# Optimization experiments

Hardware: AMD Instinct MI355X
Metric: run time of the kernel (lower is better)

Reference implementation:

```python
import jax, jax.numpy as jnp
import numpy as np

N_NODES = 100000
N_EDGES = 3200000
HID = 16
MP_ROUNDS = 3


def _mlp(w1, b1, w2, b2, x):
    # channels-first MLP applied per edge/node: x is [C_in, E]
    h = jax.nn.relu(w1 @ x + b1[:, None])
    return w2 @ h + b2[:, None]


def setup_inputs() -> dict:
    key = jax.random.key(0)
    ks = jax.random.split(key, 20)
    s = lambda k, shp: jax.random.normal(k, shp, dtype=jnp.float32) * 0.1
    inp = {
        "nodes": jax.random.normal(ks[0], (N_NODES,), dtype=jnp.float32),
        "edges_init": jax.random.normal(ks[1], (N_EDGES,), dtype=jnp.float32),
        "senders": jax.random.randint(ks[2], (N_EDGES,), 0, N_NODES, dtype=jnp.int32),
        "receivers": jax.random.randint(ks[3], (N_EDGES,), 0, N_NODES, dtype=jnp.int32),
        # EdgeEncoder: 1 -> HID -> HID
        "enc_w1": s(ks[4], (HID, 1)), "enc_b1": jnp.zeros((HID,), jnp.float32),
        "enc_w2": s(ks[5], (HID, HID)), "enc_b2": jnp.zeros((HID,), jnp.float32),
        # Node update MLP: (1 + 2*HID) -> HID -> 1  (shared across rounds)
        "node_w1": s(ks[6], (HID, 1 + 2 * HID)), "node_b1": jnp.zeros((HID,), jnp.float32),
        "node_w2": s(ks[7], (1, HID)), "node_b2": jnp.zeros((1,), jnp.float32),
        # Edge update MLP: (HID + 2) -> HID -> HID  (shared across rounds)
        "edge_w1": s(ks[8], (HID, HID + 2)), "edge_b1": jnp.zeros((HID,), jnp.float32),
        "edge_w2": s(ks[9], (HID, HID)), "edge_b2": jnp.zeros((HID,), jnp.float32),
        # EdgeDecoder: HID -> HID -> 1
        "dec_w1": s(ks[10], (HID, HID)), "dec_b1": jnp.zeros((HID,), jnp.float32),
        "dec_w2": s(ks[11], (1, HID)), "dec_b2": jnp.zeros((1,), jnp.float32),
        "alpha": jnp.float32(0.1),
    }
    return inp


def reference(nodes, edges_init, senders, receivers,
              enc_w1, enc_b1, enc_w2, enc_b2,
              node_w1, node_b1, node_w2, node_b2,
              edge_w1, edge_b1, edge_w2, edge_b2,
              dec_w1, dec_b1, dec_w2, dec_b2, alpha):
    n_nodes = nodes.shape[0]
    norm = jnp.abs(edges_init).max()
    e = edges_init / norm                      # [E]
    e = _mlp(enc_w1, enc_b1, enc_w2, enc_b2, e[None, :])   # [HID, E]
    for _ in range(MP_ROUNDS):                 # shared-weight MP blocks
        # gather/scatter: aggregate edge features to nodes
        agg_s = jax.ops.segment_sum(e.T, senders, num_segments=n_nodes).T     # [HID, N]
        agg_r = jax.ops.segment_sum(e.T, receivers, num_segments=n_nodes).T   # [HID, N]
        node_in = jnp.concatenate([nodes[None, :], agg_s, agg_r], axis=0)     # [1+2H, N]
        nodes = _mlp(node_w1, node_b1, node_w2, node_b2, node_in)[0]          # [N]
        edge_in = jnp.concatenate([e, nodes[senders][None, :], nodes[receivers][None, :]], axis=0)  # [H+2, E]
        e = _mlp(edge_w1, edge_b1, edge_w2, edge_b2, edge_in)                 # [HID, E]
    e = _mlp(dec_w1, dec_b1, dec_w2, dec_b2, e)[0]          # [E]
    low_tri_data = edges_init + alpha * (e * norm)          # L = L + alpha*GNN(L)
    return low_tri_data
```

## Files before the change

kernel.cpp:

```cpp
#include <hip/hip_runtime.h>
#include <hip/hip_bf16.h>

#define N_NODES 100000
#define N_EDGES 3200000
#define HID 16
#define NB 256
#define NPB 391
#define SCAP 15360
#define RCAP 15360
#define FDEPTH 32
#define LCAP1 8704
#define LCAP2 26624

static constexpr int BLK = 256;

__device__ __forceinline__ float frelu(float x) { return fmaxf(x, 0.f); }
__device__ __forceinline__ float bflo(unsigned int u) {
  return __uint_as_float(u << 16);
}
__device__ __forceinline__ float bfhi(unsigned int u) {
  return __uint_as_float(u & 0xFFFF0000u);
}

union E16 {
  float4 f4[2];
  __hip_bfloat16 h[16];
};

__global__ __launch_bounds__(256) void k_norm(const float* __restrict__ edges,
                                              unsigned int* __restrict__ normbits) {
  float m = 0.f;
  for (int i = blockIdx.x * blockDim.x + threadIdx.x; i < N_EDGES;
       i += gridDim.x * blockDim.x)
    m = fmaxf(m, fabsf(edges[i]));
#pragma unroll
  for (int off = 32; off > 0; off >>= 1)
    m = fmaxf(m, __shfl_down(m, off, 64));
  __shared__ float smax[BLK / 64];
  if ((threadIdx.x & 63) == 0) smax[threadIdx.x >> 6] = m;
  __syncthreads();
  if (threadIdx.x == 0) {
    float b = smax[0];
#pragma unroll
    for (int w = 1; w < BLK / 64; ++w) b = fmaxf(b, smax[w]);
    atomicMax(normbits, __float_as_uint(b));
  }
}

__global__ __launch_bounds__(1024) void k_split(
    const int* __restrict__ senders, const int* __restrict__ receivers,
    const float* __restrict__ edges, int* __restrict__ gcnt,
    unsigned int* __restrict__ pM, float* __restrict__ pV,
    unsigned int* __restrict__ pO) {
  __shared__ __align__(16) unsigned int fM[NB][FDEPTH];
  __shared__ __align__(16) unsigned int fV[NB][FDEPTH];
  __shared__ __align__(16) unsigned int fO[NB][FDEPTH];
  __shared__ int fcnt[NB];
  const int t = threadIdx.x;
  if (t < NB) fcnt[t] = 0;
  __syncthreads();
  const int e0 = blockIdx.x * (N_EDGES / 256);
  const int e1 = e0 + (N_EDGES / 256);
  for (int base = e0; base < e1; base += 1024) {
    const int i = base + t;
    if (i < e1) {
      int s = senders[i];
      unsigned int b = (unsigned int)s / NPB;
      unsigned int m = (((unsigned int)s - b * NPB) << 22) | (unsigned int)i;
      unsigned int v = __float_as_uint(edges[i]);
      unsigned int o = (unsigned int)receivers[i];
      int pos = atomicAdd(&fcnt[b], 1);
      if (pos < FDEPTH) {
        fM[b][pos] = m; fV[b][pos] = v; fO[b][pos] = o;
      } else {
        int gb = atomicAdd(&gcnt[b], 1);
        if (gb < SCAP) {
          pM[(size_t)b * SCAP + gb] = m;
          pV[(size_t)b * SCAP + gb] = __uint_as_float(v);
          pO[(size_t)b * SCAP + gb] = o;
        }
      }
    }
    __syncthreads();
    const bool last = (base + 1024 >= e1);
    if (t < NB) {
      int c = fcnt[t]; if (c > FDEPTH) c = FDEPTH;
      int nf = last ? c : (c & ~15);
      if (nf > 0) {
        int gb = atomicAdd(&gcnt[t], nf);
        size_t db = (size_t)t * SCAP + gb;
        if ((gb & 3) == 0 && gb + nf <= SCAP) {
          int k = 0;
          for (; k + 4 <= nf; k += 4) {
            *(uint4*)(pM + db + k) = *(const uint4*)(&fM[t][k]);
            *(uint4*)((unsigned int*)pV + db + k) = *(const uint4*)(&fV[t][k]);
            *(uint4*)(pO + db + k) = *(const uint4*)(&fO[t][k]);
          }
          for (; k < nf; ++k) {
            pM[db + k] = fM[t][k]; pV[db + k] = __uint_as_float(fV[t][k]);
            pO[db + k] = fO[t][k];
          }
        } else {
          for (int k = 0; k < nf; ++k)
            if (gb + k < SCAP) {
              pM[db + k] = fM[t][k]; pV[db + k] = __uint_as_float(fV[t][k]);
              pO[db + k] = fO[t][k];
            }
        }
        int res = c - nf;
        for (int k = 0; k < res; ++k) {
          fM[t][k] = fM[t][nf + k]; fV[t][k] = fV[t][nf + k];
          fO[t][k] = fO[t][nf + k];
        }
        fcnt[t] = res;
      } else fcnt[t] = c;
    }
    __syncthreads();
  }
}

__global__ __launch_bounds__(1024) void k_bsort1(
    const unsigned int* __restrict__ pM, const float* __restrict__ pV,
    const unsigned int* __restrict__ pO, const int* __restrict__ gcnt,
    unsigned int* __restrict__ srecv, unsigned int* __restrict__ sorig,
    float* __restrict__ sval, int* __restrict__ soff) {
  __shared__ unsigned int sM[LCAP1];
  __shared__ float sV[LCAP1];
  __shared__ unsigned int sO[LCAP1];
  __shared__ int hist[NPB], pref[NPB + 1], sc[NPB], cur[NPB];
  __shared__ int bb[NB];
  __shared__ int base_s;
  const int b = blockIdx.x, t = threadIdx.x, nt = blockDim.x;
  if (t < NB) { int c = gcnt[t]; bb[t] = c > SCAP ? SCAP : c; }
  for (int k = t; k < NPB; k += nt) hist[k] = 0;
  __syncthreads();
  if (t == 0) { int s = 0; for (int k = 0; k < b; ++k) s += bb[k]; base_s = s; }
  int nb = gcnt[b]; if (nb > SCAP) nb = SCAP;
  const unsigned int* PM = pM + (size_t)b * SCAP;
  const float* PV = pV + (size_t)b * SCAP;
  const unsigned int* PO = pO + (size_t)b * SCAP;
  for (int i = t; i < nb; i += nt) atomicAdd(&hist[PM[i] >> 22], 1);
  __syncthreads();
  if (t < NPB) sc[t] = hist[t];
  __syncthreads();
  for (int d = 1; d < NPB; d <<= 1) {
    int add = 0;
    if (t < NPB && t >= d) add = sc[t - d];
    __syncthreads();
    if (t < NPB && t >= d) sc[t] += add;
    __syncthreads();
  }
  if (t < NPB) pref[t] = sc[t] - hist[t];
  if (t == 0) pref[NPB] = sc[NPB - 1];
  __syncthreads();
  const int base = base_s;
  const int node0 = b * NPB;
  for (int k = t; k < NPB; k += nt) {
    int n = node0 + k;
    if (n < N_NODES) soff[n] = base + pref[k];
  }
  if (b == NB - 1 && t == 0) soff[N_NODES] = base + nb;
  __syncthreads();
  int klo = 0;
  while (klo < NPB) {
    int base0 = pref[klo];
    int khi = klo;
    while (khi < NPB && pref[khi + 1] - base0 <= LCAP1) ++khi;
    if (khi == klo) khi = klo + 1;
    for (int k = klo + t; k < khi; k += nt) cur[k] = pref[k];
    __syncthreads();
    for (int i = t; i < nb; i += nt) {
      unsigned int m = PM[i];
      int key = (int)(m >> 22);
      if (key >= klo && key < khi) {
        int p = atomicAdd(&cur[key], 1) - base0;
        if (p < LCAP1) { sM[p] = m; sV[p] = PV[i]; sO[p] = PO[i]; }
      }
    }
    __syncthreads();
    int csz = pref[khi] - base0;
    for (int i = t; i < csz; i += nt) {
      int g = base + base0 + i;
      srecv[g] = sO[i]; sorig[g] = sM[i] & 0x3FFFFFu; sval[g] = sV[i];
    }
    __syncthreads();
    klo = khi;
  }
}

__global__ __launch_bounds__(1024) void k_rsplit(
    const unsigned int* __restrict__ srecv, int* __restrict__ gcnt2,
    unsigned int* __restrict__ rpA) {
  __shared__ __align__(16) unsigned int fA[NB][FDEPTH];
  __shared__ int fcnt[NB];
  const int t = threadIdx.x;
  if (t < NB) fcnt[t] = 0;
  __syncthreads();
  const int e0 = blockIdx.x * (N_EDGES / 256);
  const int e1 = e0 + (N_EDGES / 256);
  for (int base = e0; base < e1; base += 1024) {
    const int i = base + t;
    if (i < e1) {
      unsigned int r = srecv[i];
      unsigned int b = r / NPB;
      unsigned int a = ((r - b * NPB) << 22) | (unsigned int)i;
      int pos = atomicAdd(&fcnt[b], 1);
      if (pos < FDEPTH) {
        fA[b][pos] = a;
      } else {
        int gb = atomicAdd(&gcnt2[b], 1);
        if (gb < RCAP) rpA[(size_t)b * RCAP + gb] = a;
      }
    }
    __syncthreads();
    const bool last = (base + 1024 >= e1);
    if (t < NB) {
      int c = fcnt[t]; if (c > FDEPTH) c = FDEPTH;
      int nf = last ? c : (c & ~15);
      if (nf > 0) {
        int gb = atomicAdd(&gcnt2[t], nf);
        size_t db = (size_t)t * RCAP + gb;
        if ((gb & 3) == 0 && gb + nf <= RCAP) {
          int k = 0;
          for (; k + 4 <= nf; k += 4)
            *(uint4*)(rpA + db + k) = *(const uint4*)(&fA[t][k]);
          for (; k < nf; ++k) rpA[db + k] = fA[t][k];
        } else {
          for (int k = 0; k < nf; ++k)
            if (gb + k < RCAP) rpA[db + k] = fA[t][k];
        }
        int res = c - nf;
        for (int k = 0; k < res; ++k) fA[t][k] = fA[t][nf + k];
        fcnt[t] = res;
      } else fcnt[t] = c;
    }
    __syncthreads();
  }
}

__global__ __launch_bounds__(1024) void k_rsort(
    const unsigned int* __restrict__ rpA, const int* __restrict__ gcnt2,
    unsigned int* __restrict__ rlist, int* __restrict__ roff) {
  __shared__ unsigned int sA[LCAP2];
  __shared__ int hist[NPB], pref[NPB + 1], sc[NPB], cur[NPB];
  __shared__ int bb[NB];
  __shared__ int base_s;
  const int b = blockIdx.x, t = threadIdx.x, nt = blockDim.x;
  if (t < NB) { int c = gcnt2[t]; bb[t] = c > RCAP ? RCAP : c; }
  for (int k = t; k < NPB; k += nt) hist[k] = 0;
  __syncthreads();
  if (t == 0) { int s = 0; for (int k = 0; k < b; ++k) s += bb[k]; base_s = s; }
  int nb = gcnt2[b]; if (nb > RCAP) nb = RCAP;
  const unsigned int* PA = rpA + (size_t)b * RCAP;
  for (int i = t; i < nb; i += nt) atomicAdd(&hist[PA[i] >> 22], 1);
  __syncthreads();
  if (t < NPB) sc[t] = hist[t];
  __syncthreads();
  for (int d = 1; d < NPB; d <<= 1) {
    int add = 0;
    if (t < NPB && t >= d) add = sc[t - d];
    __syncthreads();
    if (t < NPB && t >= d) sc[t] += add;
    __syncthreads();
  }
  if (t < NPB) pref[t] = sc[t] - hist[t];
  if (t == 0) pref[NPB] = sc[NPB - 1];
  __syncthreads();
  const int base = base_s;
  const int node0 = b * NPB;
  for (int k = t; k < NPB; k += nt) {
    int n = node0 + k;
    if (n < N_NODES) roff[n] = base + pref[k];
  }
  if (b == NB - 1 && t == 0) roff[N_NODES] = base + nb;
  __syncthreads();
  int klo = 0;
  while (klo < NPB) {
    int base0 = pref[klo];
    int khi = klo;
    while (khi < NPB && pref[khi + 1] - base0 <= LCAP2) ++khi;
    if (khi == klo) khi = klo + 1;
    for (int k = klo + t; k < khi; k += nt) cur[k] = pref[k];
    __syncthreads();
    for (int i = t; i < nb; i += nt) {
      unsigned int a = PA[i];
      int key = (int)(a >> 22);
      if (key >= klo && key < khi) {
        int p = atomicAdd(&cur[key], 1) - base0;
        if (p < LCAP2) sA[p] = a;
      }
    }
    __syncthreads();
    int csz = pref[khi] - base0;
    for (int i = t; i < csz; i += nt)
      rlist[base + base0 + i] = sA[i] & 0x3FFFFFu;
    __syncthreads();
    klo = khi;
  }
}

__global__ __launch_bounds__(256) void k_encode(
    const float* __restrict__ sval, const float* __restrict__ w1,
    const float* __restrict__ b1, const float* __restrict__ w2,
    const float* __restrict__ b2, const unsigned int* __restrict__ normbits,
    unsigned short* __restrict__ e) {
  int i = blockIdx.x * blockDim.x + threadIdx.x;
  float norm = __uint_as_float(*normbits);
  float x = sval[i] / norm;
  float h[HID];
#pragma unroll
  for (int j = 0; j < HID; ++j) h[j] = frelu(fmaf(w1[j], x, b1[j]));
  E16 o;
#pragma unroll
  for (int j = 0; j < HID; ++j) {
    float acc = b2[j];
#pragma unroll
    for (int k = 0; k < HID; ++k) acc = fmaf(w2[j * HID + k], h[k], acc);
    o.h[j] = __float2bfloat16(acc);
  }
  float4* ep = (float4*)(e + (size_t)i * HID);
  ep[0] = o.f4[0];
  ep[1] = o.f4[1];
}

__global__ __launch_bounds__(256) void k_aggR(
    const unsigned short* __restrict__ e, const int* __restrict__ roff,
    const unsigned int* __restrict__ rlist, float* __restrict__ aggR) {
  int wave = (blockIdx.x * blockDim.x + threadIdx.x) >> 6;
  int lane = threadIdx.x & 63, half = lane >> 5, l32 = lane & 31;
  int sub = l32 & 1, j16 = l32 >> 1;
  int n = wave * 2 + half;
  int r0 = roff[n], rdeg = roff[n + 1] - r0;
  float acc[8] = {0, 0, 0, 0, 0, 0, 0, 0};
  for (int s0 = 0; s0 < rdeg; s0 += 16) {
    int slot = s0 + j16;
    bool ok = slot < rdeg;
    int idx = r0 + (ok ? slot : 0);
    unsigned int si = rlist[idx];
    uint4 raw = *(const uint4*)(e + (size_t)si * HID + sub * 8);
    float v[8] = {bflo(raw.x), bfhi(raw.x), bflo(raw.y), bfhi(raw.y),
                  bflo(raw.z), bfhi(raw.z), bflo(raw.w), bfhi(raw.w)};
#pragma unroll
    for (int c = 0; c < 8; ++c) acc[c] += ok ? v[c] : 0.f;
  }
#pragma unroll
  for (int off = 16; off >= 2; off >>= 1)
#pragma unroll
    for (int c = 0; c < 8; ++c) acc[c] += __shfl_down(acc[c], off, 64);
  if (l32 < 2) {
    *(float4*)(aggR + (size_t)n * 16 + sub * 8) =
        make_float4(acc[0], acc[1], acc[2], acc[3]);
    *(float4*)(aggR + (size_t)n * 16 + sub * 8 + 4) =
        make_float4(acc[4], acc[5], acc[6], acc[7]);
  }
}

__global__ __launch_bounds__(256) void k_nodeup(
    const unsigned short* __restrict__ e, const int* __restrict__ soff,
    const float* __restrict__ aggR, const float* __restrict__ nodesr,
    const float* __restrict__ nw1, const float* __restrict__ nb1_,
    const float* __restrict__ nw2, const float* __restrict__ nb2_,
    float* __restrict__ nodesw) {
  int wave = (blockIdx.x * blockDim.x + threadIdx.x) >> 6;
  int lane = threadIdx.x & 63, half = lane >> 5, l32 = lane & 31;
  int n = wave * 2 + half;
  int s0 = soff[n], sdeg = soff[n + 1] - s0;
  float nsv = nodesr[n];
  float accS[16];
#pragma unroll
  for (int c = 0; c < 16; ++c) accS[c] = 0.f;
  for (int c0 = 0; c0 < sdeg; c0 += 32) {
    int k = c0 + l32;
    bool ok = k < sdeg;
    int idx = s0 + (ok ? k : 0);
    uint4 ra = *(const uint4*)(e + (size_t)idx * HID);
    uint4 rb = *(const uint4*)(e + (size_t)idx * HID + 8);
    float x[16] = {bflo(ra.x), bfhi(ra.x), bflo(ra.y), bfhi(ra.y),
                   bflo(ra.z), bfhi(ra.z), bflo(ra.w), bfhi(ra.w),
                   bflo(rb.x), bfhi(rb.x), bflo(rb.y), bfhi(rb.y),
                   bflo(rb.z), bfhi(rb.z), bflo(rb.w), bfhi(rb.w)};
#pragma unroll
    for (int c = 0; c < 16; ++c) accS[c] += ok ? x[c] : 0.f;
  }
#pragma unroll
  for (int off = 16; off >= 1; off >>= 1)
#pragma unroll
    for (int c = 0; c < 16; ++c) accS[c] += __shfl_down(accS[c], off, 64);
  float aS[16];
#pragma unroll
  for (int c = 0; c < 16; ++c) aS[c] = __shfl(accS[c], half * 32, 64);
  float pv = 0.f;
  if (l32 < 16) {
    int j = l32;
    float a1 = fmaf(nw1[j * 33], nsv, nb1_[j]);
#pragma unroll
    for (int k = 0; k < 16; ++k) a1 = fmaf(nw1[j * 33 + 1 + k], aS[k], a1);
#pragma unroll
    for (int k = 0; k < 16; ++k)
      a1 = fmaf(nw1[j * 33 + 17 + k], aggR[(size_t)n * 16 + k], a1);
    pv = nw2[j] * frelu(a1);
  }
#pragma unroll
  for (int off = 8; off >= 1; off >>= 1) pv += __shfl_down(pv, off, 64);
  if (l32 == 0) nodesw[n] = pv + nb2_[0];
}

__global__ __launch_bounds__(256) void k_edgeN(
    unsigned short* __restrict__ e, const int* __restrict__ soff,
    const unsigned int* __restrict__ srecv, const float* __restrict__ nodes,
    const float* __restrict__ w1, const float* __restrict__ b1,
    const float* __restrict__ w2, const float* __restrict__ b2) {
  int wave = (blockIdx.x * blockDim.x + threadIdx.x) >> 6;
  int lane = threadIdx.x & 63, half = lane >> 5, l32 = lane & 31;
  int n = wave * 2 + half;
  int s0 = soff[n], sdeg = soff[n + 1] - s0;
  float nsv = nodes[n];
  for (int c0 = 0; c0 < sdeg; c0 += 32) {
    int k = c0 + l32;
    bool ok = k < sdeg;
    int idx = s0 + (ok ? k : 0);
    uint4 ra = *(const uint4*)(e + (size_t)idx * HID);
    uint4 rb = *(const uint4*)(e + (size_t)idx * HID + 8);
    float x[16] = {bflo(ra.x), bfhi(ra.x), bflo(ra.y), bfhi(ra.y),
                   bflo(ra.z), bfhi(ra.z), bflo(ra.w), bfhi(ra.w),
                   bflo(rb.x), bfhi(rb.x), bflo(rb.y), bfhi(rb.y),
                   bflo(rb.z), bfhi(rb.z), bflo(rb.w), bfhi(rb.w)};
    float nrv = nodes[srecv[idx]];
    float h[16];
#pragma unroll
    for (int j = 0; j < 16; ++j) {
      float a1 = b1[j];
#pragma unroll
      for (int kk = 0; kk < 16; ++kk) a1 = fmaf(w1[j * 18 + kk], x[kk], a1);
      a1 = fmaf(w1[j * 18 + 16], nsv, a1);
      a1 = fmaf(w1[j * 18 + 17], nrv, a1);
      h[j] = frelu(a1);
    }
    E16 o;
#pragma unroll
    for (int c = 0; c < 16; ++c) {
      float a2 = b2[c];
#pragma unroll
      for (int j = 0; j < 16; ++j) a2 = fmaf(w2[c * HID + j], h[j], a2);
      o.h[c] = __float2bfloat16(a2);
    }
    if (ok) {
      *(float4*)(e + (size_t)idx * HID) = o.f4[0];
      *(float4*)(e + (size_t)idx * HID + 8) = o.f4[1];
    }
  }
}

__global__ __launch_bounds__(256) void k_final(
    const unsigned short* __restrict__ e, const int* __restrict__ soff,
    const unsigned int* __restrict__ srecv, const unsigned int* __restrict__ sorig,
    const float* __restrict__ sval, const float* __restrict__ nodes,
    const float* __restrict__ ew1, const float* __restrict__ eb1,
    const float* __restrict__ ew2, const float* __restrict__ eb2,
    const float* __restrict__ dw1, const float* __restrict__ db1,
    const float* __restrict__ dw2, const float* __restrict__ db2,
    const unsigned int* __restrict__ normbits, const float* __restrict__ alpha,
    float* __restrict__ out) {
  int wave = (blockIdx.x * blockDim.x + threadIdx.x) >> 6;
  int lane = threadIdx.x & 63, half = lane >> 5, l32 = lane & 31;
  int n = wave * 2 + half;
  int s0 = soff[n], sdeg = soff[n + 1] - s0;
  float nsv = nodes[n];
  float alphaN = alpha[0] * __uint_as_float(*normbits);
  for (int c0 = 0; c0 < sdeg; c0 += 32) {
    int k = c0 + l32;
    bool ok = k < sdeg;
    int idx = s0 + (ok ? k : 0);
    uint4 ra = *(const uint4*)(e + (size_t)idx * HID);
    uint4 rb = *(const uint4*)(e + (size_t)idx * HID + 8);
    float x[16] = {bflo(ra.x), bfhi(ra.x), bflo(ra.y), bfhi(ra.y),
                   bflo(ra.z), bfhi(ra.z), bflo(ra.w), bfhi(ra.w),
                   bflo(rb.x), bfhi(rb.x), bflo(rb.y), bfhi(rb.y),
                   bflo(rb.z), bfhi(rb.z), bflo(rb.w), bfhi(rb.w)};
    float nrv = nodes[srecv[idx]];
    float h[16];
#pragma unroll
    for (int j = 0; j < 16; ++j) {
      float a1 = eb1[j];
#pragma unroll
      for (int kk = 0; kk < 16; ++kk) a1 = fmaf(ew1[j * 18 + kk], x[kk], a1);
      a1 = fmaf(ew1[j * 18 + 16], nsv, a1);
      a1 = fmaf(ew1[j * 18 + 17], nrv, a1);
      h[j] = frelu(a1);
    }
    float y[16];
#pragma unroll
    for (int c = 0; c < 16; ++c) {
      float a2 = eb2[c];
#pragma unroll
      for (int j = 0; j < 16; ++j) a2 = fmaf(ew2[c * HID + j], h[j], a2);
      y[c] = a2;
    }
    float d = db2[0];
#pragma unroll
    for (int j = 0; j < 16; ++j) {
      float a1 = db1[j];
#pragma unroll
      for (int kk = 0; kk < 16; ++kk) a1 = fmaf(dw1[j * HID + kk], y[kk], a1);
      d = fmaf(dw2[j], frelu(a1), d);
    }
    if (ok) out[sorig[idx]] = fmaf(alphaN, d, sval[idx]);
  }
}

extern "C" void kernel_launch(void* const* d_in, const int* in_sizes, int n_in,
                              void* d_out, int out_size, void* d_ws,
                              size_t ws_size, hipStream_t stream) {
  const float* nodes0 = (const float*)d_in[0];
  const float* edges0 = (const float*)d_in[1];
  const int* senders = (const int*)d_in[2];
  const int* receivers = (const int*)d_in[3];
  const float* enc_w1 = (const float*)d_in[4];
  const float* enc_b1 = (const float*)d_in[5];
  const float* enc_w2 = (const float*)d_in[6];
  const float* enc_b2 = (const float*)d_in[7];
  const float* node_w1 = (const float*)d_in[8];
  const float* node_b1 = (const float*)d_in[9];
  const float* node_w2 = (const float*)d_in[10];
  const float* node_b2 = (const float*)d_in[11];
  const float* edge_w1 = (const float*)d_in[12];
  const float* edge_b1 = (const float*)d_in[13];
  const float* edge_w2 = (const float*)d_in[14];
  const float* edge_b2 = (const float*)d_in[15];
  const float* dec_w1 = (const float*)d_in[16];
  const float* dec_b1 = (const float*)d_in[17];
  const float* dec_w2 = (const float*)d_in[18];
  const float* dec_b2 = (const float*)d_in[19];
  const float* alpha = (const float*)d_in[20];

  char* ws = (char*)d_ws;
  unsigned short* e = (unsigned short*)ws;
  char* p = ws + (size_t)N_EDGES * HID * 2;
  unsigned int* srecv = (unsigned int*)p;  p += (size_t)N_EDGES * 4;
  unsigned int* sorig = (unsigned int*)p;  p += (size_t)N_EDGES * 4;
  float* sval = (float*)p;                 p += (size_t)N_EDGES * 4;
  unsigned int* rlist = (unsigned int*)p;  p += (size_t)N_EDGES * 4;
  float* aggR = (float*)p;                 p += (size_t)N_NODES * 16 * 4;
  int* soff = (int*)p;                     p += (size_t)(N_NODES + 16) * 4;
  int* roff = (int*)p;                     p += (size_t)(N_NODES + 16) * 4;
  float* nbA = (float*)p;                  p += (size_t)N_NODES * 4;
  float* nbB = (float*)p;                  p += (size_t)N_NODES * 4;
  unsigned int* normbits = (unsigned int*)p; p += 64;
  int* gcnt = (int*)p;                     p += NB * 4;
  int* gcnt2 = (int*)p;                    p += NB * 4;
  unsigned int* pM = (unsigned int*)ws;
  float* pV = (float*)(ws + (size_t)NB * SCAP * 4);
  unsigned int* pO = (unsigned int*)(ws + (size_t)NB * SCAP * 8);
  unsigned int* rpA = (unsigned int*)(ws + (size_t)NB * SCAP * 12);

  const int ngrid = 12500;
  const int egrid = N_EDGES / BLK;

  hipMemsetAsync(normbits, 0, 64 + 2 * NB * 4, stream);
  k_norm<<<512, BLK, 0, stream>>>(edges0, normbits);
  k_split<<<256, 1024, 0, stream>>>(senders, receivers, edges0, gcnt, pM, pV, pO);
  k_bsort1<<<NB, 1024, 0, stream>>>(pM, pV, pO, gcnt, srecv, sorig, sval, soff);
  k_rsplit<<<256, 1024, 0, stream>>>(srecv, gcnt2, rpA);
  k_rsort<<<NB, 1024, 0, stream>>>(rpA, gcnt2, rlist, roff);
  k_encode<<<egrid, BLK, 0, stream>>>(sval, enc_w1, enc_b1, enc_w2, enc_b2,
                                      normbits, e);
  k_aggR<<<ngrid, BLK, 0, stream>>>(e, roff, rlist, aggR);
  k_nodeup<<<ngrid, BLK, 0, stream>>>(e, soff, aggR, nodes0, node_w1, node_b1,
                                      node_w2, node_b2, nbA);
  k_edgeN<<<ngrid, BLK, 0, stream>>>(e, soff, srecv, nbA, edge_w1, edge_b1,
                                     edge_w2, edge_b2);
  k_aggR<<<ngrid, BLK, 0, stream>>>(e, roff, rlist, aggR);
  k_nodeup<<<ngrid, BLK, 0, stream>>>(e, soff, aggR, nbA, node_w1, node_b1,
                                      node_w2, node_b2, nbB);
  k_edgeN<<<ngrid, BLK, 0, stream>>>(e, soff, srecv, nbB, edge_w1, edge_b1,
                                     edge_w2, edge_b2);
  k_aggR<<<ngrid, BLK, 0, stream>>>(e, roff, rlist, aggR);
  k_nodeup<<<ngrid, BLK, 0, stream>>>(e, soff, aggR, nbB, node_w1, node_b1,
                                      node_w2, node_b2, nbA);
  k_final<<<ngrid, BLK, 0, stream>>>(e, soff, srecv, sorig, sval, nbA, edge_w1,
                                     edge_b1, edge_w2, edge_b2, dec_w1, dec_b1,
                                     dec_w2, dec_b2, normbits, alpha,
                                     (float*)d_out);
}
```

Baseline: 1.057 ms.

## Switch edge-update and final kernels from per-node waves to per-edge threads

```diff
diff --git a/kernel.cpp b/kernel.cpp
--- a/kernel.cpp
+++ b/kernel.cpp
@@ -20,6 +20,17 @@
 }
 __device__ __forceinline__ float bfhi(unsigned int u) {
   return __uint_as_float(u & 0xFFFF0000u);
+}
+
+__device__ __forceinline__ int find_bucket(const int* __restrict__ bstart,
+                                           int i) {
+  int lo = 0, hi = NB;
+#pragma unroll
+  for (int s = 0; s < 8; ++s) {
+    int mid = (lo + hi) >> 1;
+    if (i >= bstart[mid]) lo = mid; else hi = mid;
+  }
+  return lo;
 }
 
 union E16 {
@@ -123,7 +134,8 @@
     const unsigned int* __restrict__ pM, const float* __restrict__ pV,
     const unsigned int* __restrict__ pO, const int* __restrict__ gcnt,
     unsigned int* __restrict__ srecv, unsigned int* __restrict__ sorig,
-    float* __restrict__ sval, int* __restrict__ soff) {
+    unsigned short* __restrict__ svalbf, int* __restrict__ soff,
+    int* __restrict__ bstart) {
   __shared__ unsigned int sM[LCAP1];
   __shared__ float sV[LCAP1];
   __shared__ unsigned int sO[LCAP1];
@@ -159,7 +171,11 @@
     int n = node0 + k;
     if (n < N_NODES) soff[n] = base + pref[k];
   }
-  if (b == NB - 1 && t == 0) soff[N_NODES] = base + nb;
+  if (t == 0) bstart[b] = base;
+  if (b == NB - 1 && t == 0) {
+    soff[N_NODES] = base + nb;
+    bstart[NB] = base + nb;
+  }
   __syncthreads();
   int klo = 0;
   while (klo < NPB) {
@@ -181,11 +197,23 @@
     int csz = pref[khi] - base0;
     for (int i = t; i < csz; i += nt) {
       int g = base + base0 + i;
-      srecv[g] = sO[i]; sorig[g] = sM[i] & 0x3FFFFFu; sval[g] = sV[i];
+      srecv[g] = sO[i]; sorig[g] = sM[i] & 0x3FFFFFu;
+      __hip_bfloat16 hb = __float2bfloat16(sV[i]);
+      svalbf[g] = *(unsigned short*)&hb;
     }
     __syncthreads();
     klo = khi;
   }
+}
+
+__global__ __launch_bounds__(256) void k_sfill(
+    const int* __restrict__ soff, unsigned short* __restrict__ ssend16) {
+  int wave = (blockIdx.x * blockDim.x + threadIdx.x) >> 6;
+  int lane = threadIdx.x & 63, half = lane >> 5, l32 = lane & 31;
+  int n = wave * 2 + half;
+  unsigned short local = (unsigned short)(n - (n / NPB) * NPB);
+  int s0 = soff[n], s1 = soff[n + 1];
+  for (int k = s0 + l32; k < s1; k += 32) ssend16[k] = local;
 }
 
 __global__ __launch_bounds__(1024) void k_rsplit(
@@ -300,13 +328,13 @@
 }
 
 __global__ __launch_bounds__(256) void k_encode(
-    const float* __restrict__ sval, const float* __restrict__ w1,
+    const unsigned short* __restrict__ svalbf, const float* __restrict__ w1,
     const float* __restrict__ b1, const float* __restrict__ w2,
     const float* __restrict__ b2, const unsigned int* __restrict__ normbits,
     unsigned short* __restrict__ e) {
   int i = blockIdx.x * blockDim.x + threadIdx.x;
   float norm = __uint_as_float(*normbits);
-  float x = sval[i] / norm;
+  float x = bflo((unsigned int)svalbf[i]) / norm;
   float h[HID];
 #pragma unroll
   for (int j = 0; j < HID; ++j) h[j] = frelu(fmaf(w1[j], x, b1[j]));
@@ -405,107 +433,100 @@
   if (l32 == 0) nodesw[n] = pv + nb2_[0];
 }
 
-__global__ __launch_bounds__(256) void k_edgeN(
-    unsigned short* __restrict__ e, const int* __restrict__ soff,
-    const unsigned int* __restrict__ srecv, const float* __restrict__ nodes,
-    const float* __restrict__ w1, const float* __restrict__ b1,
-    const float* __restrict__ w2, const float* __restrict__ b2) {
-  int wave = (blockIdx.x * blockDim.x + threadIdx.x) >> 6;
-  int lane = threadIdx.x & 63, half = lane >> 5, l32 = lane & 31;
-  int n = wave * 2 + half;
-  int s0 = soff[n], sdeg = soff[n + 1] - s0;
-  float nsv = nodes[n];
-  for (int c0 = 0; c0 < sdeg; c0 += 32) {
-    int k = c0 + l32;
-    bool ok = k < sdeg;
-    int idx = s0 + (ok ? k : 0);
-    uint4 ra = *(const uint4*)(e + (size_t)idx * HID);
-    uint4 rb = *(const uint4*)(e + (size_t)idx * HID + 8);
-    float x[16] = {bflo(ra.x), bfhi(ra.x), bflo(ra.y), bfhi(ra.y),
-                   bflo(ra.z), bfhi(ra.z), bflo(ra.w), bfhi(ra.w),
-                   bflo(rb.x), bfhi(rb.x), bflo(rb.y), bfhi(rb.y),
-                   bflo(rb.z), bfhi(rb.z), bflo(rb.w), bfhi(rb.w)};
-    float nrv = nodes[srecv[idx]];
-    float h[16];
-#pragma unroll
-    for (int j = 0; j < 16; ++j) {
-      float a1 = b1[j];
-#pragma unroll
-      for (int kk = 0; kk < 16; ++kk) a1 = fmaf(w1[j * 18 + kk], x[kk], a1);
-      a1 = fmaf(w1[j * 18 + 16], nsv, a1);
-      a1 = fmaf(w1[j * 18 + 17], nrv, a1);
-      h[j] = frelu(a1);
-    }
-    E16 o;
-#pragma unroll
-    for (int c = 0; c < 16; ++c) {
-      float a2 = b2[c];
-#pragma unroll
-      for (int j = 0; j < 16; ++j) a2 = fmaf(w2[c * HID + j], h[j], a2);
-      o.h[c] = __float2bfloat16(a2);
-    }
-    if (ok) {
-      *(float4*)(e + (size_t)idx * HID) = o.f4[0];
-      *(float4*)(e + (size_t)idx * HID + 8) = o.f4[1];
-    }
-  }
-}
-
-__global__ __launch_bounds__(256) void k_final(
-    const unsigned short* __restrict__ e, const int* __restrict__ soff,
-    const unsigned int* __restrict__ srecv, const unsigned int* __restrict__ sorig,
-    const float* __restrict__ sval, const float* __restrict__ nodes,
+__global__ __launch_bounds__(256, 4) void k_edgeE(
+    unsigned short* __restrict__ e, const unsigned int* __restrict__ srecv,
+    const unsigned short* __restrict__ ssend16, const int* __restrict__ bstart,
+    const float* __restrict__ nodes, const float* __restrict__ w1,
+    const float* __restrict__ b1, const float* __restrict__ w2,
+    const float* __restrict__ b2) {
+  int i = blockIdx.x * blockDim.x + threadIdx.x;
+  int bk = find_bucket(bstart, i);
+  int snd = bk * NPB + (int)ssend16[i];
+  float ns = nodes[snd], nr = nodes[srecv[i]];
+  float4* ep = (float4*)(e + (size_t)i * HID);
+  E16 in;
+  in.f4[0] = ep[0];
+  in.f4[1] = ep[1];
+  float x[HID];
+#pragma unroll
+  for (int k = 0; k < HID; ++k) x[k] = __bfloat162float(in.h[k]);
+  float h[HID];
+#pragma unroll
+  for (int j = 0; j < HID; ++j) {
+    float acc = b1[j];
+#pragma unroll
+    for (int k = 0; k < HID; ++k) acc = fmaf(w1[j * 18 + k], x[k], acc);
+    acc = fmaf(w1[j * 18 + 16], ns, acc);
+    acc = fmaf(w1[j * 18 + 17], nr, acc);
+    h[j] = frelu(acc);
+  }
+  E16 o;
+#pragma unroll
+  for (int j = 0; j < HID; ++j) {
+    float acc = b2[j];
+#pragma unroll
+    for (int k = 0; k < HID; ++k) acc = fmaf(w2[j * HID + k], h[k], acc);
+    o.h[j] = __float2bfloat16(acc);
+  }
+  ep[0] = o.f4[0];
+  ep[1] = o.f4[1];
+}
+
+__global__ __launch_bounds__(256, 4) void k_final(
+    const unsigned short* __restrict__ e, const unsigned int* __restrict__ srecv,
+    const unsigned short* __restrict__ ssend16, const int* __restrict__ bstart,
+    const unsigned int* __restrict__ sorig, const float* __restrict__ nodes,
     const float* __restrict__ ew1, const float* __restrict__ eb1,
     const float* __restrict__ ew2, const float* __restrict__ eb2,
     const float* __restrict__ dw1, const float* __restrict__ db1,
     const float* __restrict__ dw2, const float* __restrict__ db2,
     const unsigned int* __restrict__ normbits, const float* __restrict__ alpha,
     float* __restrict__ out) {
-  int wave = (blockIdx.x * blockDim.x + threadIdx.x) >> 6;
-  int lane = threadIdx.x & 63, half = lane >> 5, l32 = lane & 31;
-  int n = wave * 2 + half;
-  int s0 = soff[n], sdeg = soff[n + 1] - s0;
-  float nsv = nodes[n];
+  int i = blockIdx.x * blockDim.x + threadIdx.x;
+  int bk = find_bucket(bstart, i);
+  int snd = bk * NPB + (int)ssend16[i];
+  float ns = nodes[snd], nr = nodes[srecv[i]];
+  const float4* ep = (const float4*)(e + (size_t)i * HID);
+  E16 in;
+  in.f4[0] = ep[0];
+  in.f4[1] = ep[1];
+  float x[HID];
+#pragma unroll
+  for (int k = 0; k < HID; ++k) x[k] = __bfloat162float(in.h[k]);
+  float h[HID];
+#pragma unroll
+  for (int j = 0; j < HID; ++j) {
+    float acc = eb1[j];
+#pragma unroll
+    for (int k = 0; k < HID; ++k) acc = fmaf(ew1[j * 18 + k], x[k], acc);
+    acc = fmaf(ew1[j * 18 + 16], ns, acc);
+    acc = fmaf(ew1[j * 18 + 17], nr, acc);
+    h[j] = frelu(acc);
+  }
+  float y[HID];
+#pragma unroll
+  for (int j = 0; j < HID; ++j) {
+    float acc = eb2[j];
+#pragma unroll
+    for (int k = 0; k < HID; ++k) acc = fmaf(ew2[j * HID + k], h[k], acc);
+    y[j] = acc;
+  }
+  float d = db2[0];
+#pragma unroll
+  for (int j = 0; j < HID; ++j) {
+    float acc = db1[j];
+#pragma unroll
+    for (int k = 0; k < HID; ++k) acc = fmaf(dw1[j * HID + k], y[k], acc);
+    d = fmaf(dw2[j], frelu(acc), d);
+  }
   float alphaN = alpha[0] * __uint_as_float(*normbits);
-  for (int c0 = 0; c0 < sdeg; c0 += 32) {
-    int k = c0 + l32;
-    bool ok = k < sdeg;
-    int idx = s0 + (ok ? k : 0);
-    uint4 ra = *(const uint4*)(e + (size_t)idx * HID);
-    uint4 rb = *(const uint4*)(e + (size_t)idx * HID + 8);
-    float x[16] = {bflo(ra.x), bfhi(ra.x), bflo(ra.y), bfhi(ra.y),
-                   bflo(ra.z), bfhi(ra.z), bflo(ra.w), bfhi(ra.w),
-                   bflo(rb.x), bfhi(rb.x), bflo(rb.y), bfhi(rb.y),
-                   bflo(rb.z), bfhi(rb.z), bflo(rb.w), bfhi(rb.w)};
-    float nrv = nodes[srecv[idx]];
-    float h[16];
-#pragma unroll
-    for (int j = 0; j < 16; ++j) {
-      float a1 = eb1[j];
-#pragma unroll
-      for (int kk = 0; kk < 16; ++kk) a1 = fmaf(ew1[j * 18 + kk], x[kk], a1);
-      a1 = fmaf(ew1[j * 18 + 16], nsv, a1);
-      a1 = fmaf(ew1[j * 18 + 17], nrv, a1);
-      h[j] = frelu(a1);
-    }
-    float y[16];
-#pragma unroll
-    for (int c = 0; c < 16; ++c) {
-      float a2 = eb2[c];
-#pragma unroll
-      for (int j = 0; j < 16; ++j) a2 = fmaf(ew2[c * HID + j], h[j], a2);
-      y[c] = a2;
-    }
-    float d = db2[0];
-#pragma unroll
-    for (int j = 0; j < 16; ++j) {
-      float a1 = db1[j];
-#pragma unroll
-      for (int kk = 0; kk < 16; ++kk) a1 = fmaf(dw1[j * HID + kk], y[kk], a1);
-      d = fmaf(dw2[j], frelu(a1), d);
-    }
-    if (ok) out[sorig[idx]] = fmaf(alphaN, d, sval[idx]);
-  }
+  out[sorig[i]] = alphaN * d;
+}
+
+__global__ __launch_bounds__(256) void k_resid(const float* __restrict__ edges,
+                                               float* __restrict__ out) {
+  int i = blockIdx.x * blockDim.x + threadIdx.x;
+  out[i] += edges[i];
 }
 
 extern "C" void kernel_launch(void* const* d_in, const int* in_sizes, int n_in,
@@ -536,18 +557,20 @@
   char* ws = (char*)d_ws;
   unsigned short* e = (unsigned short*)ws;
   char* p = ws + (size_t)N_EDGES * HID * 2;
-  unsigned int* srecv = (unsigned int*)p;  p += (size_t)N_EDGES * 4;
-  unsigned int* sorig = (unsigned int*)p;  p += (size_t)N_EDGES * 4;
-  float* sval = (float*)p;                 p += (size_t)N_EDGES * 4;
-  unsigned int* rlist = (unsigned int*)p;  p += (size_t)N_EDGES * 4;
-  float* aggR = (float*)p;                 p += (size_t)N_NODES * 16 * 4;
-  int* soff = (int*)p;                     p += (size_t)(N_NODES + 16) * 4;
-  int* roff = (int*)p;                     p += (size_t)(N_NODES + 16) * 4;
-  float* nbA = (float*)p;                  p += (size_t)N_NODES * 4;
-  float* nbB = (float*)p;                  p += (size_t)N_NODES * 4;
+  unsigned int* srecv = (unsigned int*)p;    p += (size_t)N_EDGES * 4;
+  unsigned int* sorig = (unsigned int*)p;    p += (size_t)N_EDGES * 4;
+  unsigned int* rlist = (unsigned int*)p;    p += (size_t)N_EDGES * 4;
+  unsigned short* ssend16 = (unsigned short*)p; p += (size_t)N_EDGES * 2;
+  unsigned short* svalbf = (unsigned short*)p;  p += (size_t)N_EDGES * 2;
+  float* aggR = (float*)p;                   p += (size_t)N_NODES * 16 * 4;
+  int* soff = (int*)p;                       p += (size_t)(N_NODES + 16) * 4;
+  int* roff = (int*)p;                       p += (size_t)(N_NODES + 16) * 4;
+  float* nbA = (float*)p;                    p += (size_t)N_NODES * 4;
+  float* nbB = (float*)p;                    p += (size_t)N_NODES * 4;
   unsigned int* normbits = (unsigned int*)p; p += 64;
-  int* gcnt = (int*)p;                     p += NB * 4;
-  int* gcnt2 = (int*)p;                    p += NB * 4;
+  int* gcnt = (int*)p;                       p += NB * 4;
+  int* gcnt2 = (int*)p;                      p += NB * 4;
+  int* bstart = (int*)p;                     p += (NB + 1) * 4;
   unsigned int* pM = (unsigned int*)ws;
   float* pV = (float*)(ws + (size_t)NB * SCAP * 4);
   unsigned int* pO = (unsigned int*)(ws + (size_t)NB * SCAP * 8);
@@ -559,26 +582,29 @@
   hipMemsetAsync(normbits, 0, 64 + 2 * NB * 4, stream);
   k_norm<<<512, BLK, 0, stream>>>(edges0, normbits);
   k_split<<<256, 1024, 0, stream>>>(senders, receivers, edges0, gcnt, pM, pV, pO);
-  k_bsort1<<<NB, 1024, 0, stream>>>(pM, pV, pO, gcnt, srecv, sorig, sval, soff);
+  k_bsort1<<<NB, 1024, 0, stream>>>(pM, pV, pO, gcnt, srecv, sorig, svalbf,
+                                    soff, bstart);
+  k_sfill<<<ngrid, BLK, 0, stream>>>(soff, ssend16);
   k_rsplit<<<256, 1024, 0, stream>>>(srecv, gcnt2, rpA);
   k_rsort<<<NB, 1024, 0, stream>>>(rpA, gcnt2, rlist, roff);
-  k_encode<<<egrid, BLK, 0, stream>>>(sval, enc_w1, enc_b1, enc_w2, enc_b2,
+  k_encode<<<egrid, BLK, 0, stream>>>(svalbf, enc_w1, enc_b1, enc_w2, enc_b2,
                                       normbits, e);
   k_aggR<<<ngrid, BLK, 0, stream>>>(e, roff, rlist, aggR);
   k_nodeup<<<ngrid, BLK, 0, stream>>>(e, soff, aggR, nodes0, node_w1, node_b1,
                                       node_w2, node_b2, nbA);
-  k_edgeN<<<ngrid, BLK, 0, stream>>>(e, soff, srecv, nbA, edge_w1, edge_b1,
-                                     edge_w2, edge_b2);
+  k_edgeE<<<egrid, BLK, 0, stream>>>(e, srecv, ssend16, bstart, nbA, edge_w1,
+                                     edge_b1, edge_w2, edge_b2);
   k_aggR<<<ngrid, BLK, 0, stream>>>(e, roff, rlist, aggR);
   k_nodeup<<<ngrid, BLK, 0, stream>>>(e, soff, aggR, nbA, node_w1, node_b1,
                                       node_w2, node_b2, nbB);
-  k_edgeN<<<ngrid, BLK, 0, stream>>>(e, soff, srecv, nbB, edge_w1, edge_b1,
-                                     edge_w2, edge_b2);
+  k_edgeE<<<egrid, BLK, 0, stream>>>(e, srecv, ssend16, bstart, nbB, edge_w1,
+                                     edge_b1, edge_w2, edge_b2);
   k_aggR<<<ngrid, BLK, 0, stream>>>(e, roff, rlist, aggR);
   k_nodeup<<<ngrid, BLK, 0, stream>>>(e, soff, aggR, nbB, node_w1, node_b1,
                                       node_w2, node_b2, nbA);
-  k_final<<<ngrid, BLK, 0, stream>>>(e, soff, srecv, sorig, sval, nbA, edge_w1,
-                                     edge_b1, edge_w2, edge_b2, dec_w1, dec_b1,
-                                     dec_w2, dec_b2, normbits, alpha,
-                                     (float*)d_out);
-}
+  k_final<<<egrid, BLK, 0, stream>>>(e, srecv, ssend16, bstart, sorig, nbA,
+                                     edge_w1, edge_b1, edge_w2, edge_b2,
+                                     dec_w1, dec_b1, dec_w2, dec_b2, normbits,
+                                     alpha, (float*)d_out);
+  k_resid<<<egrid, BLK, 0, stream>>>(edges0, (float*)d_out);
+}
```

After: 993.8 us. 1.06x faster.
